# Optimization experiments

Measured on AMD Instinct MI355X. Metric: run time of the kernel, lower is better.

## Reference

```python
import jax, jax.numpy as jnp
import numpy as np

MEM = 32      # mem_size == slot_size (required by role/mem einsum contraction)
SLOT = 32
NREAD = 1
NITER = 3
NIN = 3       # num_input
EPS = 1e-8


def _ln(x, g=None, b=None, eps=1e-5):
    m = x.mean(-1, keepdims=True)
    v = x.var(-1, keepdims=True)
    y = (x - m) / jnp.sqrt(v + eps)
    if g is not None:
        y = y * g + b
    return y


def _lstm_layer(x, Wih, Whh, bih, bhh):
    # x: [S, B, Din]; torch gate order i, f, g, o
    B = x.shape[1]
    H = Whh.shape[1]
    def step(carry, xt):
        h, c = carry
        z = xt @ Wih.T + h @ Whh.T + bih + bhh
        i, f, g, o = jnp.split(z, 4, axis=-1)
        c = jax.nn.sigmoid(f) * c + jax.nn.sigmoid(i) * jnp.tanh(g)
        h = jax.nn.sigmoid(o) * jnp.tanh(c)
        return (h, c), h
    init = (jnp.zeros((B, H), x.dtype), jnp.zeros((B, H), x.dtype))
    _, hs = jax.lax.scan(step, init, x)
    return hs


def _slot_attention(inp, inp_cat, Wi, bi, Wq, bq, Wk, bk, Wv, bv, lng, lnb,
                    Wm1, bm1, Wm2, bm2, Wsp, bsp):
    # inp: [S, B, NIN, 64]; dropout is identity (eval)
    S, B = inp.shape[0], inp.shape[1]
    init_slots = (inp_cat @ Wi.T + bi).reshape(S, B, -1, SLOT)
    k = jax.nn.elu(inp @ Wk.T + bk) + 1.0
    v = inp @ Wv.T + bv
    slots = init_slots
    for _ in range(NITER):
        q = (slots @ Wq.T + bq + init_slots) * SLOT ** (-0.5)
        q = jax.nn.elu(q) + 1.0
        logits = jnp.einsum('sbik,sbjk->sbij', k, q)
        attn = jax.nn.softmax(logits, axis=3) + EPS
        attn = attn / attn.sum(axis=2, keepdims=True)
        upd = jnp.einsum('sbij,sbik->sbjk', attn, v)
        h = _ln(upd, lng, lnb)
        mlp = jax.nn.relu(h @ Wm1.T + bm1) @ Wm2.T + bm2
        slots = slots + mlp / SLOT
    slots = jnp.concatenate([init_slots, slots], axis=-1)
    return slots @ Wsp.T + bsp


def _mask_read(slots, mask, i):
    return jnp.tanh(jnp.einsum('sbne,n->sbe', slots, jnp.roll(mask, i)))


def setup_inputs() -> dict:
    key = jax.random.key(0)
    ks = jax.random.split(key, 20)
    def n(k, shape):
        return jax.random.normal(k, shape, jnp.float32) * 0.05
    z = lambda s: jnp.zeros(s, jnp.float32)
    return {
        'tokens': jax.random.randint(ks[0], (512, 64), 0, 32000),
        'embed_W': n(ks[1], (32000, 256)),
        'Wih0': n(ks[2], (2048, 256)), 'Whh0': n(ks[3], (2048, 512)),
        'bih0': z(2048), 'bhh0': z(2048),
        'Wih1': n(ks[4], (2048, 512)), 'Whh1': n(ks[5], (2048, 512)),
        'bih1': z(2048), 'bhh1': z(2048),
        'Wpi': n(ks[6], (192, 256)), 'bpi': z(192),
        'Wq': n(ks[7], (32, 32)), 'bq': z(32),
        'Wk': n(ks[8], (32, 64)), 'bk': z(32),
        'Wv': n(ks[9], (32, 64)), 'bv': z(32),
        'lng': jnp.ones(32, jnp.float32), 'lnb': z(32),
        'Wm1': n(ks[10], (64, 32)), 'bm1': z(64),
        'Wm2': n(ks[11], (32, 64)), 'bm2': z(32),
        'Wbind': n(ks[12], (96, 192)), 'bbind': z(96),
        'Wreas': n(ks[13], (64, 192)), 'breas': z(64),
        'Wsp': n(ks[14], (32, 64)), 'bsp': z(32),
        'Wg': n(ks[15], (1, 512)), 'bg': z(1),
        'Wout': n(ks[16], (128, 544)), 'bout': z(128),
    }


def reference(tokens, embed_W, Wih0, Whh0, bih0, bhh0, Wih1, Whh1, bih1, bhh1,
              Wpi, bpi, Wq, bq, Wk, bk, Wv, bv, lng, lnb, Wm1, bm1, Wm2, bm2,
              Wbind, bbind, Wreas, breas, Wsp, bsp, Wg, bg, Wout, bout):
    S, B = tokens.shape
    emb = embed_W[tokens]                                   # [S,B,256]
    h = _lstm_layer(emb, Wih0, Whh0, bih0, bhh0)            # [S,B,512]
    h = _lstm_layer(h, Wih1, Whh1, bih1, bhh1)
    dec_in = (emb @ Wpi.T + bpi).reshape(S, B, NIN, -1)     # [S,B,3,64]
    dec_cat = dec_in.reshape(S, B, -1)
    sa = (Wq, bq, Wk, bk, Wv, bv, lng, lnb, Wm1, bm1, Wm2, bm2, Wsp, bsp)
    bind_slots = _slot_attention(dec_in, dec_cat, Wbind, bbind, *sa)  # [S,B,3,32]
    reas_slots = _slot_attention(dec_in, dec_cat, Wreas, breas, *sa)  # [S,B,2,32]
    e = 1e-6
    mask_b = jnp.array([1.0 - 2 * e, e, e], emb.dtype)
    role1 = _mask_read(bind_slots, mask_b, 0)
    role2 = _mask_read(bind_slots, mask_b, 1)
    filler = _mask_read(bind_slots, mask_b, 2)
    mask_r = jnp.array([1.0 - (1 + NREAD) * e, e], emb.dtype)
    u1 = _mask_read(reas_slots, mask_r, 0)
    u2 = _mask_read(reas_slots, mask_r, 1)
    gate = jax.nn.sigmoid(h @ Wg.T + bg + 1.0)              # [S,B,1]

    def step(mem, xs):
        r1, r2, f, g_t, u1t, u2t = xs
        role = jnp.einsum('br,bt->brt', r1, r2)
        prev = jnp.einsum('brt,brtf->bf', role, mem)
        cur = g_t * (f - prev)
        mem = mem + jnp.einsum('brt,bf->brtf', role, cur / MEM)
        nrm = jnp.sqrt(jnp.sum(mem * mem, axis=(1, 2, 3)))
        nrm = jax.nn.relu(nrm - 1.0) + 1.0
        mem = mem / nrm[:, None, None, None]
        read = _ln(jnp.einsum('bsrv,bs,br->bv', mem, u1t, u2t))
        return mem, read

    mem0 = jnp.zeros((B, MEM, MEM, MEM), emb.dtype)
    _, reads = jax.lax.scan(step, mem0, (role1, role2, filler, gate, u1, u2))
    out = jnp.concatenate([h, reads], axis=-1) @ Wout.T + bout
    return out
```

## Files before the change

### kernel.cpp

```cpp
#include <hip/hip_runtime.h>

typedef unsigned short u16;
typedef unsigned int u32;
typedef unsigned long long u64;
typedef __bf16 bf16x8 __attribute__((ext_vector_type(8)));
typedef float f32x4 __attribute__((ext_vector_type(4)));

__device__ __forceinline__ float bf2f(u16 u) { return __uint_as_float(((u32)u) << 16); }
__device__ __forceinline__ u16 f2bf(float f) {
    u32 u = __float_as_uint(f);
    u32 r = (u + 0x7FFFu + ((u >> 16) & 1u)) >> 16;
    return (u16)r;
}
__device__ __forceinline__ float sigm(float x) { return 1.0f / (1.0f + __expf(-x)); }
__device__ __forceinline__ float elu1(float x) { return x > 0.0f ? x + 1.0f : __expf(x); }

__device__ __forceinline__ int ag_load(const int* p) {
    return __hip_atomic_load(p, __ATOMIC_RELAXED, __HIP_MEMORY_SCOPE_AGENT);
}
__device__ __forceinline__ void ag_store(int* p, int v) {
    __hip_atomic_store(p, v, __ATOMIC_RELAXED, __HIP_MEMORY_SCOPE_AGENT);
}
__device__ __forceinline__ void llc_store2(u16* p, u16 a, u16 b) {
    u32 v = (u32)a | ((u32)b << 16);
    __hip_atomic_store((u32*)p, v, __ATOMIC_RELAXED, __HIP_MEMORY_SCOPE_AGENT);
}
__device__ __forceinline__ void llc_store_u16(u16* p, u16 v) {
    __hip_atomic_store(p, v, __ATOMIC_RELAXED, __HIP_MEMORY_SCOPE_AGENT);
}

struct Cvt8 { const float* s[8]; u16* d[8]; int off4[9]; };

__global__ __launch_bounds__(256) void k_f2b8(Cvt8 c)
{
    int i = blockIdx.x * 256 + threadIdx.x;
    if (i >= c.off4[8]) return;
    int k = 0;
#pragma unroll
    for (int q = 1; q < 8; q++) if (i >= c.off4[q]) k = q;
    int j = i - c.off4[k];
    float4 v = ((const float4*)c.s[k])[j];
    ushort4 o;
    o.x = f2bf(v.x); o.y = f2bf(v.y); o.z = f2bf(v.z); o.w = f2bf(v.w);
    ((ushort4*)c.d[k])[j] = o;
}

__global__ __launch_bounds__(256) void k_embed(const int* __restrict__ tok,
                                               const float* __restrict__ W,
                                               u16* __restrict__ out)
{
    int c = blockIdx.x * 256 + threadIdx.x;
    int row = c >> 5, cc = (c & 31) * 8;
    int t = tok[row];
    const float* src = W + (size_t)t * 256 + cc;
    u16 tmp[8];
#pragma unroll
    for (int k = 0; k < 8; k++) tmp[k] = f2bf(src[k]);
    *(uint4*)(out + (size_t)row * 256 + cc) = *(uint4*)tmp;
}

__global__ __launch_bounds__(256) void k_gemm_bt(
    const u16* __restrict__ A, int lda,
    const u16* __restrict__ B,
    u16* __restrict__ Cb, float* __restrict__ Cf, int ldc,
    const float* __restrict__ bias1, const float* __restrict__ bias2,
    int N, int K)
{
    __shared__ u16 As[128][40];
    __shared__ u16 Bs[128][40];
    const int tid = threadIdx.x;
    const int m0 = blockIdx.x * 128, n0 = blockIdx.y * 128;
    const int wave = tid >> 6, lane = tid & 63;
    const int wm = wave & 1, wn = wave >> 1;
    const int quad = lane >> 4, l16 = lane & 15;
    f32x4 acc[4][4] = {};
    for (int k0 = 0; k0 < K; k0 += 32) {
        __syncthreads();
#pragma unroll
        for (int i = 0; i < 2; i++) {
            int c = tid + i * 256, row = c >> 2, cc = (c & 3) * 8;
            *(uint4*)(&As[row][cc]) = *(const uint4*)(A + (size_t)(m0 + row) * lda + k0 + cc);
            uint4 d = {0, 0, 0, 0};
            if (n0 + row < N) d = *(const uint4*)(B + (size_t)(n0 + row) * K + k0 + cc);
            *(uint4*)(&Bs[row][cc]) = d;
        }
        __syncthreads();
        bf16x8 af[4], bfm[4];
#pragma unroll
        for (int x = 0; x < 4; x++) {
            af[x]  = *(const bf16x8*)(&As[wm * 64 + x * 16 + l16][quad * 8]);
            bfm[x] = *(const bf16x8*)(&Bs[wn * 64 + x * 16 + l16][quad * 8]);
        }
#pragma unroll
        for (int mi = 0; mi < 4; mi++)
#pragma unroll
            for (int ni = 0; ni < 4; ni++)
                acc[mi][ni] = __builtin_amdgcn_mfma_f32_16x16x32_bf16(af[mi], bfm[ni], acc[mi][ni], 0, 0, 0);
    }
#pragma unroll
    for (int ni = 0; ni < 4; ni++) {
        int col = n0 + wn * 64 + ni * 16 + l16;
        if (col < N) {
            float bv = 0.f;
            if (bias1) bv += bias1[col];
            if (bias2) bv += bias2[col];
#pragma unroll
            for (int mi = 0; mi < 4; mi++) {
                int r0 = m0 + wm * 64 + mi * 16 + quad * 4;
#pragma unroll
                for (int r = 0; r < 4; r++) {
                    float v = acc[mi][ni][r] + bv;
                    if (Cb) Cb[(size_t)(r0 + r) * ldc + col] = f2bf(v);
                    else    Cf[(size_t)(r0 + r) * ldc + col] = v;
                }
            }
        }
    }
}

template <int NSLOT>
__global__ __launch_bounds__(256) void k_slot(
    const u16* __restrict__ dec, const u16* __restrict__ initp,
    const float* __restrict__ Wq, const float* __restrict__ bq,
    const float* __restrict__ Wk, const float* __restrict__ bk,
    const float* __restrict__ Wv, const float* __restrict__ bv,
    const float* __restrict__ lng, const float* __restrict__ lnb,
    const float* __restrict__ Wm1, const float* __restrict__ bm1,
    const float* __restrict__ Wm2, const float* __restrict__ bm2,
    const float* __restrict__ Wsp, const float* __restrict__ bsp,
    float* __restrict__ o1, float* __restrict__ o2, float* __restrict__ o3)
{
    __shared__ float WqT[32][33], WkT[64][33], WvT[64][33], Wm1T[32][65], Wm2T[64][33], WspT[64][33];
    __shared__ float bq_s[32], bk_s[32], bv_s[32], bm1_s[64], bm2_s[32], bsp_s[32], g_s[32], be_s[32];
    __shared__ u16 xbuf[8][192];
    __shared__ float slots[8][3][32], initl[8][3][32], kk[8][3][32], vv[8][3][32], qq[8][3][32];
    __shared__ float att[8][3][4];
    __shared__ float ubuf[8][32];
    __shared__ float hid[8][64];
    const int tid = threadIdx.x;
    for (int i = tid; i < 1024; i += 256) { int o = i >> 5, c = i & 31; WqT[c][o] = Wq[o * 32 + c]; }
    for (int i = tid; i < 2048; i += 256) {
        int o6 = i >> 6, c6 = i & 63;
        WkT[c6][o6]  = Wk[o6 * 64 + c6];
        WvT[c6][o6]  = Wv[o6 * 64 + c6];
        Wm2T[c6][o6] = Wm2[o6 * 64 + c6];
        WspT[c6][o6] = Wsp[o6 * 64 + c6];
        int o5 = i >> 5, c5 = i & 31;
        Wm1T[c5][o5] = Wm1[o5 * 32 + c5];
    }
    if (tid < 32) {
        bq_s[tid] = bq[tid]; bk_s[tid] = bk[tid]; bv_s[tid] = bv[tid];
        bm2_s[tid] = bm2[tid]; bsp_s[tid] = bsp[tid];
        g_s[tid] = lng[tid]; be_s[tid] = lnb[tid];
    }
    if (tid < 64) bm1_s[tid] = bm1[tid];
    const int p = tid >> 5, l = tid & 31;
    const size_t row = (size_t)blockIdx.x * 8 + p;
    for (int i = l; i < 192; i += 32) xbuf[p][i] = dec[row * 192 + i];
    __syncthreads();
#pragma unroll
    for (int i = 0; i < 3; i++) {
        float aK = bk_s[l], aV = bv_s[l];
        for (int c = 0; c < 64; c++) {
            float x = bf2f(xbuf[p][i * 64 + c]);
            aK += x * WkT[c][l];
            aV += x * WvT[c][l];
        }
        kk[p][i][l] = elu1(aK);
        vv[p][i][l] = aV;
    }
#pragma unroll
    for (int j = 0; j < NSLOT; j++) {
        float iv = bf2f(initp[row * (NSLOT * 32) + j * 32 + l]);
        initl[p][j][l] = iv;
        slots[p][j][l] = iv;
    }
    __syncthreads();
    const float rs = 0.17677669529663687f;
    for (int it = 0; it < 3; it++) {
#pragma unroll
        for (int j = 0; j < NSLOT; j++) {
            float a = bq_s[l];
            for (int c = 0; c < 32; c++) a += slots[p][j][c] * WqT[c][l];
            qq[p][j][l] = elu1((a + initl[p][j][l]) * rs);
        }
        __syncthreads();
        if (l < 3 * NSLOT) {
            int i = l / NSLOT, j = l % NSLOT;
            float s = 0.f;
            for (int c = 0; c < 32; c++) s += kk[p][i][c] * qq[p][j][c];
            att[p][i][j] = s;
        }
        __syncthreads();
        if (l < 3) {
            float mx = -1e30f;
            for (int j = 0; j < NSLOT; j++) mx = fmaxf(mx, att[p][l][j]);
            float sm = 0.f, ex[NSLOT];
            for (int j = 0; j < NSLOT; j++) { ex[j] = __expf(att[p][l][j] - mx); sm += ex[j]; }
            for (int j = 0; j < NSLOT; j++) att[p][l][j] = ex[j] / sm + 1e-8f;
        }
        __syncthreads();
        if (l < NSLOT) {
            float s = att[p][0][l] + att[p][1][l] + att[p][2][l];
            float inv = 1.0f / s;
            for (int i = 0; i < 3; i++) att[p][i][l] *= inv;
        }
        __syncthreads();
#pragma unroll
        for (int j = 0; j < NSLOT; j++) {
            float u = att[p][0][j] * vv[p][0][l] + att[p][1][j] * vv[p][1][l] + att[p][2][j] * vv[p][2][l];
            float mean = u;
            for (int mk = 1; mk < 32; mk <<= 1) mean += __shfl_xor(mean, mk, 32);
            mean *= (1.0f / 32.0f);
            float d = u - mean;
            float var = d * d;
            for (int mk = 1; mk < 32; mk <<= 1) var += __shfl_xor(var, mk, 32);
            var *= (1.0f / 32.0f);
            float y = d * rsqrtf(var + 1e-5f) * g_s[l] + be_s[l];
            ubuf[p][l] = y;
            __syncthreads();
#pragma unroll
            for (int oo = 0; oo < 2; oo++) {
                int o = l + oo * 32;
                float a = bm1_s[o];
                for (int c = 0; c < 32; c++) a += ubuf[p][c] * Wm1T[c][o];
                hid[p][o] = fmaxf(a, 0.f);
            }
            __syncthreads();
            float a2 = bm2_s[l];
            for (int c = 0; c < 64; c++) a2 += hid[p][c] * Wm2T[c][l];
            slots[p][j][l] += a2 * (1.0f / 32.0f);
            __syncthreads();
        }
    }
    float pj[NSLOT];
#pragma unroll
    for (int j = 0; j < NSLOT; j++) {
        float a = bsp_s[l];
        for (int c = 0; c < 32; c++) a += initl[p][j][c] * WspT[c][l];
        for (int c = 0; c < 32; c++) a += slots[p][j][c] * WspT[32 + c][l];
        pj[j] = a;
    }
    const float e = 1e-6f, me = (float)(1.0 - 2e-6);
    if (NSLOT == 3) {
        o1[row * 32 + l] = tanhf(me * pj[0] + e * pj[1] + e * pj[2]);
        o2[row * 32 + l] = tanhf(e * pj[0] + me * pj[1] + e * pj[2]);
        o3[row * 32 + l] = tanhf(e * pj[0] + e * pj[1] + me * pj[2]);
    } else {
        o1[row * 32 + l] = tanhf(me * pj[0] + e * pj[1]);
        o2[row * 32 + l] = tanhf(e * pj[0] + me * pj[1]);
    }
}

__global__ __launch_bounds__(256) void k_mega(
    const u16* __restrict__ emb,
    const u16* __restrict__ Wx0, const u16* __restrict__ Wh0,
    const u16* __restrict__ Wx1, const u16* __restrict__ Wh1,
    const float* __restrict__ bi0, const float* __restrict__ bh0,
    const float* __restrict__ bi1, const float* __restrict__ bh1,
    u16* __restrict__ h0seq,
    u16* __restrict__ h1seq,
    u16* __restrict__ acat,
    int* __restrict__ flags,
    const float* __restrict__ r1, const float* __restrict__ r2,
    const float* __restrict__ fi, const float* __restrict__ uu1,
    const float* __restrict__ uu2,
    const float* __restrict__ Wg, const float* __restrict__ bg)
{
    const int tid = threadIdx.x;
    const int blk = blockIdx.x;
    int* f0  = flags;
    int* f1  = flags + 4096;
    int* f1s = flags + 8192;

    if (blk < 128) {
        __shared__ u16 Wx[32][528];
        __shared__ u16 Wh[32][528];
        __shared__ float zs[4][16][33];
        const int layer = blk >> 6;
        const int me = blk & 63;
        const int jbase = me * 8;
        const int Kx = layer ? 512 : 256;
        const u16* Wxp = layer ? Wx1 : Wx0;
        const u16* Whp = layer ? Wh1 : Wh0;
        const float* bi = layer ? bi1 : bi0;
        const float* bh = layer ? bh1 : bh0;
#pragma unroll
        for (int i = 0; i < 8; i++) {
            int c = tid + i * 256;
            int row = c >> 6, cc = (c & 63) * 8;
            int grow = (row >> 3) * 512 + jbase + (row & 7);
            *(uint4*)(&Wh[row][cc]) = *(const uint4*)(Whp + (size_t)grow * 512 + cc);
        }
        {
            int cpr = Kx >> 3;
            int iters = (32 * cpr) >> 8;
            for (int i = 0; i < iters; i++) {
                int c = tid + i * 256;
                int row = c / cpr, cc = (c % cpr) * 8;
                int grow = (row >> 3) * 512 + jbase + (row & 7);
                *(uint4*)(&Wx[row][cc]) = *(const uint4*)(Wxp + (size_t)grow * Kx + cc);
            }
        }
        const int wave = tid >> 6, lane = tid & 63;
        const int quad = lane >> 4, l16 = lane & 15;
        const int m = wave * 16 + l16;
        const int bl = lane >> 2;
        const int b = wave * 16 + bl;
        const int jj = (lane & 3) * 2;
        const int hoff = quad * 512 + m * 8;
        float bia0[4], bia1[4];
#pragma unroll
        for (int g = 0; g < 4; g++) {
            bia0[g] = bi[g * 512 + jbase + jj]     + bh[g * 512 + jbase + jj];
            bia1[g] = bi[g * 512 + jbase + jj + 1] + bh[g * 512 + jbase + jj + 1];
        }
        const int pollOwn = (wave * 64 + lane) * 16;
        const int pubIdx  = (wave * 64 + me) * 16;
        float c0 = 0.f, c1 = 0.f;
        __syncthreads();
        for (int t = 0; t < 512; t++) {
            f32x4 acc0 = {}, acc1 = {};
            if (!layer) {
                const u16* xrow = emb + ((size_t)t * 64 + m) * 256;
#pragma unroll
                for (int kc = 0; kc < 8; kc++) {
                    bf16x8 a  = *(const bf16x8*)(xrow + kc * 32 + quad * 8);
                    bf16x8 w0 = *(const bf16x8*)(&Wx[l16][kc * 32 + quad * 8]);
                    bf16x8 w1 = *(const bf16x8*)(&Wx[16 + l16][kc * 32 + quad * 8]);
                    acc0 = __builtin_amdgcn_mfma_f32_16x16x32_bf16(a, w0, acc0, 0, 0, 0);
                    acc1 = __builtin_amdgcn_mfma_f32_16x16x32_bf16(a, w1, acc1, 0, 0, 0);
                }
                if (t > 0) {
                    int it = 0;
                    for (;;) {
                        int a = ag_load(f0 + pollOwn);
                        if (__all(a >= t)) break;
                        if (++it > 3000000) break;
                        __builtin_amdgcn_s_sleep(1);
                    }
                    const u16* hrd = h0seq + (size_t)(t - 1) * 32768 + hoff;
#pragma unroll
                    for (int kc = 0; kc < 16; kc++) {
                        bf16x8 a  = *(const bf16x8*)(hrd + kc * 2048);
                        bf16x8 w0 = *(const bf16x8*)(&Wh[l16][kc * 32 + quad * 8]);
                        bf16x8 w1 = *(const bf16x8*)(&Wh[16 + l16][kc * 32 + quad * 8]);
                        acc0 = __builtin_amdgcn_mfma_f32_16x16x32_bf16(a, w0, acc0, 0, 0, 0);
                        acc1 = __builtin_amdgcn_mfma_f32_16x16x32_bf16(a, w1, acc1, 0, 0, 0);
                    }
                }
            } else {
                {
                    int it = 0;
                    for (;;) {
                        int a = ag_load(f0 + pollOwn);
                        if (__all(a >= t + 1)) break;
                        if (++it > 3000000) break;
                        __builtin_amdgcn_s_sleep(1);
                    }
                }
                const u16* xrow = h0seq + (size_t)t * 32768 + hoff;
#pragma unroll
                for (int kc = 0; kc < 16; kc++) {
                    bf16x8 a  = *(const bf16x8*)(xrow + kc * 2048);
                    bf16x8 w0 = *(const bf16x8*)(&Wx[l16][kc * 32 + quad * 8]);
                    bf16x8 w1 = *(const bf16x8*)(&Wx[16 + l16][kc * 32 + quad * 8]);
                    acc0 = __builtin_amdgcn_mfma_f32_16x16x32_bf16(a, w0, acc0, 0, 0, 0);
                    acc1 = __builtin_amdgcn_mfma_f32_16x16x32_bf16(a, w1, acc1, 0, 0, 0);
                }
                if (t > 0) {
                    int it = 0;
                    for (;;) {
                        int a = ag_load(f1 + pollOwn);
                        if (__all(a >= t)) break;
                        if (++it > 3000000) break;
                        __builtin_amdgcn_s_sleep(1);
                    }
                    const u16* hrd = h1seq + (size_t)(t - 1) * 32768 + hoff;
#pragma unroll
                    for (int kc = 0; kc < 16; kc++) {
                        bf16x8 a  = *(const bf16x8*)(hrd + kc * 2048);
                        bf16x8 w0 = *(const bf16x8*)(&Wh[l16][kc * 32 + quad * 8]);
                        bf16x8 w1 = *(const bf16x8*)(&Wh[16 + l16][kc * 32 + quad * 8]);
                        acc0 = __builtin_amdgcn_mfma_f32_16x16x32_bf16(a, w0, acc0, 0, 0, 0);
                        acc1 = __builtin_amdgcn_mfma_f32_16x16x32_bf16(a, w1, acc1, 0, 0, 0);
                    }
                }
            }
#pragma unroll
            for (int r = 0; r < 4; r++) {
                zs[wave][quad * 4 + r][l16]      = acc0[r];
                zs[wave][quad * 4 + r][16 + l16] = acc1[r];
            }
            u16 hb0, hb1;
            {
                float zi0 = zs[wave][bl][jj]      + bia0[0];
                float zf0 = zs[wave][bl][8 + jj]  + bia0[1];
                float zg0 = zs[wave][bl][16 + jj] + bia0[2];
                float zo0 = zs[wave][bl][24 + jj] + bia0[3];
                c0 = sigm(zf0) * c0 + sigm(zi0) * tanhf(zg0);
                float h0v = sigm(zo0) * tanhf(c0);
                float zi1 = zs[wave][bl][jj + 1]      + bia1[0];
                float zf1 = zs[wave][bl][8 + jj + 1]  + bia1[1];
                float zg1 = zs[wave][bl][16 + jj + 1] + bia1[2];
                float zo1 = zs[wave][bl][24 + jj + 1] + bia1[3];
                c1 = sigm(zf1) * c1 + sigm(zi1) * tanhf(zg1);
                float h1v = sigm(zo1) * tanhf(c1);
                hb0 = f2bf(h0v); hb1 = f2bf(h1v);
            }
            if (!layer) {
                llc_store2(h0seq + (size_t)t * 32768 + me * 512 + b * 8 + jj, hb0, hb1);
                __builtin_amdgcn_s_waitcnt(0);
                if (lane == 0) ag_store(f0 + pubIdx, t + 1);
            } else {
                llc_store2(h1seq + (size_t)t * 32768 + me * 512 + b * 8 + jj, hb0, hb1);
                __builtin_amdgcn_s_waitcnt(0);
                if (lane == 0) ag_store(f1 + pubIdx, t + 1);
                llc_store2(acat + ((size_t)t * 64 + b) * 544 + jbase + jj, hb0, hb1);
                __builtin_amdgcn_s_waitcnt(0);
                if (lane == 0) ag_store(f1s + pubIdx, t + 1);
            }
        }
    } else {
        const int sb = blk - 128;
        const int grp = sb >> 4;
        const int f = tid & 31, rg = tid >> 5;
        float m[4][32];
#pragma unroll
        for (int x = 0; x < 4; x++)
            for (int y = 0; y < 32; y++) m[x][y] = 0.f;
        __shared__ float r1s[32], r2s[32], fis[32], u1s[32], u2s[32];
        __shared__ float red[8][32];
        __shared__ float wred[4];
        __shared__ float gpart[4];
        float wg0 = Wg[2 * tid], wg1 = Wg[2 * tid + 1];
        float bgv = bg[0];
        for (int t = 0; t < 512; t++) {
            float pre = 0.f;
            {
                size_t base = ((size_t)t * 64 + sb) * 32;
                if (tid < 32) pre = r1[base + tid];
                else if (tid < 64) pre = r2[base + tid - 32];
                else if (tid < 96) pre = fi[base + tid - 64];
                else if (tid < 128) pre = uu1[base + tid - 96];
                else if (tid < 160) pre = uu2[base + tid - 128];
            }
            if (tid < 64) {
                int* p1 = f1s + (grp * 64 + tid) * 16;
                int it = 0;
                for (;;) {
                    int a = ag_load(p1);
                    if (__all(a >= t + 1)) break;
                    if (++it > 3000000) break;
                    __builtin_amdgcn_s_sleep(1);
                }
            }
            __syncthreads();
            if (tid < 32) r1s[tid] = pre;
            else if (tid < 64) r2s[tid - 32] = pre;
            else if (tid < 96) fis[tid - 64] = pre;
            else if (tid < 128) u1s[tid - 96] = pre;
            else if (tid < 160) u2s[tid - 128] = pre;
            {
                const u16* hr = acat + ((size_t)t * 64 + sb) * 544;
                u32 hv = *(const u32*)(hr + 2 * tid);
                float gp = bf2f((u16)hv) * wg0 + bf2f((u16)(hv >> 16)) * wg1;
                for (int mk = 1; mk < 64; mk <<= 1) gp += __shfl_xor(gp, mk, 64);
                if ((tid & 63) == 0) gpart[tid >> 6] = gp;
            }
            __syncthreads();
            float gsh = sigm(gpart[0] + gpart[1] + gpart[2] + gpart[3] + bgv + 1.0f);
            float p = 0.f;
#pragma unroll
            for (int rl = 0; rl < 4; rl++) {
                float s = 0.f;
                for (int ti = 0; ti < 32; ti++) s += r2s[ti] * m[rl][ti];
                p += r1s[rg * 4 + rl] * s;
            }
            red[rg][f] = p;
            __syncthreads();
            float prev = 0.f;
#pragma unroll
            for (int g = 0; g < 8; g++) prev += red[g][f];
            float curo = gsh * (fis[f] - prev) * (1.0f / 32.0f);
            float nsq = 0.f;
#pragma unroll
            for (int rl = 0; rl < 4; rl++) {
                float a = r1s[rg * 4 + rl] * curo;
                for (int ti = 0; ti < 32; ti++) {
                    m[rl][ti] += a * r2s[ti];
                    nsq += m[rl][ti] * m[rl][ti];
                }
            }
            for (int mk = 1; mk < 64; mk <<= 1) nsq += __shfl_xor(nsq, mk, 64);
            __syncthreads();
            if ((tid & 63) == 0) wred[tid >> 6] = nsq;
            __syncthreads();
            float nrm = sqrtf(wred[0] + wred[1] + wred[2] + wred[3]);
            float sc = nrm > 1.0f ? 1.0f / nrm : 1.0f;
            float rp = 0.f;
#pragma unroll
            for (int rl = 0; rl < 4; rl++) {
                float s = 0.f;
                for (int ti = 0; ti < 32; ti++) {
                    m[rl][ti] *= sc;
                    s += m[rl][ti] * u2s[ti];
                }
                rp += u1s[rg * 4 + rl] * s;
            }
            red[rg][f] = rp;
            __syncthreads();
            float rv = 0.f;
#pragma unroll
            for (int g = 0; g < 8; g++) rv += red[g][f];
            float mean = rv;
            for (int mk = 1; mk < 32; mk <<= 1) mean += __shfl_xor(mean, mk, 32);
            mean *= (1.0f / 32.0f);
            float d = rv - mean;
            float var = d * d;
            for (int mk = 1; mk < 32; mk <<= 1) var += __shfl_xor(var, mk, 32);
            var *= (1.0f / 32.0f);
            if (tid < 32) {
                float y = d * rsqrtf(var + 1e-5f);
                llc_store_u16(acat + ((size_t)t * 64 + sb) * 544 + 512 + f, f2bf(y));
            }
            __syncthreads();
        }
    }
}

extern "C" void kernel_launch(void* const* d_in, const int* in_sizes, int n_in,
                              void* d_out, int out_size, void* d_ws, size_t ws_size,
                              hipStream_t stream)
{
    (void)in_sizes; (void)n_in; (void)out_size; (void)ws_size;
    const int*   tokens = (const int*)d_in[0];
    const float* embW  = (const float*)d_in[1];
    const float* Wih0  = (const float*)d_in[2];
    const float* Whh0  = (const float*)d_in[3];
    const float* bih0  = (const float*)d_in[4];
    const float* bhh0  = (const float*)d_in[5];
    const float* Wih1  = (const float*)d_in[6];
    const float* Whh1  = (const float*)d_in[7];
    const float* bih1  = (const float*)d_in[8];
    const float* bhh1  = (const float*)d_in[9];
    const float* Wpi   = (const float*)d_in[10];
    const float* bpi   = (const float*)d_in[11];
    const float* Wq    = (const float*)d_in[12];
    const float* bq    = (const float*)d_in[13];
    const float* Wk    = (const float*)d_in[14];
    const float* bk    = (const float*)d_in[15];
    const float* Wv    = (const float*)d_in[16];
    const float* bv    = (const float*)d_in[17];
    const float* lng   = (const float*)d_in[18];
    const float* lnb   = (const float*)d_in[19];
    const float* Wm1   = (const float*)d_in[20];
    const float* bm1   = (const float*)d_in[21];
    const float* Wm2   = (const float*)d_in[22];
    const float* bm2   = (const float*)d_in[23];
    const float* Wbind = (const float*)d_in[24];
    const float* bbind = (const float*)d_in[25];
    const float* Wreas = (const float*)d_in[26];
    const float* breas = (const float*)d_in[27];
    const float* Wsp   = (const float*)d_in[28];
    const float* bsp   = (const float*)d_in[29];
    const float* Wg    = (const float*)d_in[30];
    const float* bg    = (const float*)d_in[31];
    const float* Wout  = (const float*)d_in[32];
    const float* bout  = (const float*)d_in[33];

    char* ws = (char*)d_ws;
    size_t off = 0;
    auto alloc = [&](size_t bytes) { size_t o = off; off += (bytes + 255) & ~(size_t)255; return o; };
    int*  flags  = (int*)(ws + alloc(16384 * 4));
    u16*  emb    = (u16*)(ws + alloc(32768ull * 256 * 2));
    u16*  dec    = (u16*)(ws + alloc(32768ull * 192 * 2));
    u16*  initb  = (u16*)(ws + alloc(32768ull * 96 * 2));
    u16*  initr  = (u16*)(ws + alloc(32768ull * 64 * 2));
    u16*  acat   = (u16*)(ws + alloc(32768ull * 544 * 2));
    u16*  h0seq  = (u16*)(ws + alloc(512ull * 64 * 512 * 2));
    u16*  h1seq  = (u16*)(ws + alloc(512ull * 64 * 512 * 2));
    float* role1 = (float*)(ws + alloc(32768ull * 32 * 4));
    float* role2 = (float*)(ws + alloc(32768ull * 32 * 4));
    float* fill  = (float*)(ws + alloc(32768ull * 32 * 4));
    float* u1v   = (float*)(ws + alloc(32768ull * 32 * 4));
    float* u2v   = (float*)(ws + alloc(32768ull * 32 * 4));
    u16* Wx0b  = (u16*)(ws + alloc(2048ull * 256 * 2));
    u16* Wh0b  = (u16*)(ws + alloc(2048ull * 512 * 2));
    u16* Wx1b  = (u16*)(ws + alloc(2048ull * 512 * 2));
    u16* Wh1b  = (u16*)(ws + alloc(2048ull * 512 * 2));
    u16* Wpib  = (u16*)(ws + alloc(192ull * 256 * 2));
    u16* Wbindb = (u16*)(ws + alloc(96ull * 192 * 2));
    u16* Wreasb = (u16*)(ws + alloc(64ull * 192 * 2));
    u16* Woutb  = (u16*)(ws + alloc(128ull * 544 * 2));

    hipMemsetAsync(flags, 0, 16384 * 4, stream);
    {
        Cvt8 c;
        const float* s[8] = {Wih0, Whh0, Wih1, Whh1, Wpi, Wbind, Wreas, Wout};
        u16* d[8] = {Wx0b, Wh0b, Wx1b, Wh1b, Wpib, Wbindb, Wreasb, Woutb};
        int n[8] = {2048 * 256, 2048 * 512, 2048 * 512, 2048 * 512,
                    192 * 256, 96 * 192, 64 * 192, 128 * 544};
        int acc = 0;
        for (int k = 0; k < 8; k++) { c.s[k] = s[k]; c.d[k] = d[k]; c.off4[k] = acc; acc += n[k] / 4; }
        c.off4[8] = acc;
        k_f2b8<<<(acc + 255) / 256, 256, 0, stream>>>(c);
    }
    k_embed<<<4096, 256, 0, stream>>>(tokens, embW, emb);
    k_gemm_bt<<<dim3(256, 2), 256, 0, stream>>>(emb, 256, Wpib, dec, nullptr, 192, bpi, nullptr, 192, 256);
    k_gemm_bt<<<dim3(256, 1), 256, 0, stream>>>(dec, 192, Wbindb, initb, nullptr, 96, bbind, nullptr, 96, 192);
    k_gemm_bt<<<dim3(256, 1), 256, 0, stream>>>(dec, 192, Wreasb, initr, nullptr, 64, breas, nullptr, 64, 192);
    k_slot<3><<<4096, 256, 0, stream>>>(dec, initb, Wq, bq, Wk, bk, Wv, bv, lng, lnb,
                                        Wm1, bm1, Wm2, bm2, Wsp, bsp, role1, role2, fill);
    k_slot<2><<<4096, 256, 0, stream>>>(dec, initr, Wq, bq, Wk, bk, Wv, bv, lng, lnb,
                                        Wm1, bm1, Wm2, bm2, Wsp, bsp, u1v, u2v, nullptr);
    k_mega<<<192, 256, 0, stream>>>(emb, Wx0b, Wh0b, Wx1b, Wh1b,
                                    bih0, bhh0, bih1, bhh1,
                                    h0seq, h1seq, acat, flags,
                                    role1, role2, fill, u1v, u2v, Wg, bg);
    k_gemm_bt<<<dim3(256, 1), 256, 0, stream>>>(acat, 544, Woutb, nullptr, (float*)d_out, 128, bout, nullptr, 128, 544);
}
```

Baseline: 3.526 ms.

## Compact flag layout, merge layer-1 flags, and split MFMA accumulator chains

Flags are packed densely (no 64-byte padding per flag), and layer 1 now publishes one flag, after both its h1 and acat stores, instead of two. Layer-1 blocks poll the layer-0 and layer-1 flags in a single combined loop before starting their step. The MFMA loops are unrolled by two with four independent accumulators, which shortens dependency chains. The denser flags may suffer false sharing when writers hit the same cache line, and merging the polls delays the input GEMM until the recurrent dependency is also ready.

```diff
diff --git a/kernel.cpp b/kernel.cpp
--- a/kernel.cpp
+++ b/kernel.cpp
@@ -269,9 +269,8 @@
 {
     const int tid = threadIdx.x;
     const int blk = blockIdx.x;
-    int* f0  = flags;
-    int* f1  = flags + 4096;
-    int* f1s = flags + 8192;
+    int* f0 = flags;
+    int* f1 = flags + 256;
 
     if (blk < 128) {
         __shared__ u16 Wx[32][528];
@@ -315,78 +314,79 @@
             bia0[g] = bi[g * 512 + jbase + jj]     + bh[g * 512 + jbase + jj];
             bia1[g] = bi[g * 512 + jbase + jj + 1] + bh[g * 512 + jbase + jj + 1];
         }
-        const int pollOwn = (wave * 64 + lane) * 16;
-        const int pubIdx  = (wave * 64 + me) * 16;
+        int* pollF0 = f0 + wave * 64 + lane;
+        int* pollF1 = f1 + wave * 64 + lane;
+        int* pubF   = (layer ? f1 : f0) + wave * 64 + me;
         float c0 = 0.f, c1 = 0.f;
         __syncthreads();
         for (int t = 0; t < 512; t++) {
-            f32x4 acc0 = {}, acc1 = {};
+            f32x4 acc0 = {}, acc1 = {}, acc2 = {}, acc3 = {};
             if (!layer) {
                 const u16* xrow = emb + ((size_t)t * 64 + m) * 256;
 #pragma unroll
-                for (int kc = 0; kc < 8; kc++) {
-                    bf16x8 a  = *(const bf16x8*)(xrow + kc * 32 + quad * 8);
-                    bf16x8 w0 = *(const bf16x8*)(&Wx[l16][kc * 32 + quad * 8]);
-                    bf16x8 w1 = *(const bf16x8*)(&Wx[16 + l16][kc * 32 + quad * 8]);
-                    acc0 = __builtin_amdgcn_mfma_f32_16x16x32_bf16(a, w0, acc0, 0, 0, 0);
-                    acc1 = __builtin_amdgcn_mfma_f32_16x16x32_bf16(a, w1, acc1, 0, 0, 0);
+                for (int kc = 0; kc < 8; kc += 2) {
+                    bf16x8 a0 = *(const bf16x8*)(xrow + kc * 32 + quad * 8);
+                    bf16x8 a1 = *(const bf16x8*)(xrow + (kc + 1) * 32 + quad * 8);
+                    acc0 = __builtin_amdgcn_mfma_f32_16x16x32_bf16(a0, *(const bf16x8*)(&Wx[l16][kc * 32 + quad * 8]), acc0, 0, 0, 0);
+                    acc1 = __builtin_amdgcn_mfma_f32_16x16x32_bf16(a0, *(const bf16x8*)(&Wx[16 + l16][kc * 32 + quad * 8]), acc1, 0, 0, 0);
+                    acc2 = __builtin_amdgcn_mfma_f32_16x16x32_bf16(a1, *(const bf16x8*)(&Wx[l16][(kc + 1) * 32 + quad * 8]), acc2, 0, 0, 0);
+                    acc3 = __builtin_amdgcn_mfma_f32_16x16x32_bf16(a1, *(const bf16x8*)(&Wx[16 + l16][(kc + 1) * 32 + quad * 8]), acc3, 0, 0, 0);
                 }
                 if (t > 0) {
                     int it = 0;
                     for (;;) {
-                        int a = ag_load(f0 + pollOwn);
+                        int a = ag_load(pollF0);
                         if (__all(a >= t)) break;
                         if (++it > 3000000) break;
                         __builtin_amdgcn_s_sleep(1);
                     }
                     const u16* hrd = h0seq + (size_t)(t - 1) * 32768 + hoff;
 #pragma unroll
-                    for (int kc = 0; kc < 16; kc++) {
-                        bf16x8 a  = *(const bf16x8*)(hrd + kc * 2048);
-                        bf16x8 w0 = *(const bf16x8*)(&Wh[l16][kc * 32 + quad * 8]);
-                        bf16x8 w1 = *(const bf16x8*)(&Wh[16 + l16][kc * 32 + quad * 8]);
-                        acc0 = __builtin_amdgcn_mfma_f32_16x16x32_bf16(a, w0, acc0, 0, 0, 0);
-                        acc1 = __builtin_amdgcn_mfma_f32_16x16x32_bf16(a, w1, acc1, 0, 0, 0);
+                    for (int kc = 0; kc < 16; kc += 2) {
+                        bf16x8 a0 = *(const bf16x8*)(hrd + kc * 2048);
+                        bf16x8 a1 = *(const bf16x8*)(hrd + (kc + 1) * 2048);
+                        acc0 = __builtin_amdgcn_mfma_f32_16x16x32_bf16(a0, *(const bf16x8*)(&Wh[l16][kc * 32 + quad * 8]), acc0, 0, 0, 0);
+                        acc1 = __builtin_amdgcn_mfma_f32_16x16x32_bf16(a0, *(const bf16x8*)(&Wh[16 + l16][kc * 32 + quad * 8]), acc1, 0, 0, 0);
+                        acc2 = __builtin_amdgcn_mfma_f32_16x16x32_bf16(a1, *(const bf16x8*)(&Wh[l16][(kc + 1) * 32 + quad * 8]), acc2, 0, 0, 0);
+                        acc3 = __builtin_amdgcn_mfma_f32_16x16x32_bf16(a1, *(const bf16x8*)(&Wh[16 + l16][(kc + 1) * 32 + quad * 8]), acc3, 0, 0, 0);
                     }
                 }
             } else {
                 {
                     int it = 0;
                     for (;;) {
-                        int a = ag_load(f0 + pollOwn);
-                        if (__all(a >= t + 1)) break;
+                        int a0 = ag_load(pollF0);
+                        int a1 = ag_load(pollF1);
+                        if (__all((a0 >= t + 1) && (a1 >= t))) break;
                         if (++it > 3000000) break;
                         __builtin_amdgcn_s_sleep(1);
                     }
                 }
                 const u16* xrow = h0seq + (size_t)t * 32768 + hoff;
 #pragma unroll
-                for (int kc = 0; kc < 16; kc++) {
-                    bf16x8 a  = *(const bf16x8*)(xrow + kc * 2048);
-                    bf16x8 w0 = *(const bf16x8*)(&Wx[l16][kc * 32 + quad * 8]);
-                    bf16x8 w1 = *(const bf16x8*)(&Wx[16 + l16][kc * 32 + quad * 8]);
-                    acc0 = __builtin_amdgcn_mfma_f32_16x16x32_bf16(a, w0, acc0, 0, 0, 0);
-                    acc1 = __builtin_amdgcn_mfma_f32_16x16x32_bf16(a, w1, acc1, 0, 0, 0);
+                for (int kc = 0; kc < 16; kc += 2) {
+                    bf16x8 a0 = *(const bf16x8*)(xrow + kc * 2048);
+                    bf16x8 a1 = *(const bf16x8*)(xrow + (kc + 1) * 2048);
+                    acc0 = __builtin_amdgcn_mfma_f32_16x16x32_bf16(a0, *(const bf16x8*)(&Wx[l16][kc * 32 + quad * 8]), acc0, 0, 0, 0);
+                    acc1 = __builtin_amdgcn_mfma_f32_16x16x32_bf16(a0, *(const bf16x8*)(&Wx[16 + l16][kc * 32 + quad * 8]), acc1, 0, 0, 0);
+                    acc2 = __builtin_amdgcn_mfma_f32_16x16x32_bf16(a1, *(const bf16x8*)(&Wx[l16][(kc + 1) * 32 + quad * 8]), acc2, 0, 0, 0);
+                    acc3 = __builtin_amdgcn_mfma_f32_16x16x32_bf16(a1, *(const bf16x8*)(&Wx[16 + l16][(kc + 1) * 32 + quad * 8]), acc3, 0, 0, 0);
                 }
                 if (t > 0) {
-                    int it = 0;
-                    for (;;) {
-                        int a = ag_load(f1 + pollOwn);
-                        if (__all(a >= t)) break;
-                        if (++it > 3000000) break;
-                        __builtin_amdgcn_s_sleep(1);
+                    const u16* hrd = h1seq + (size_t)(t - 1) * 32768 + hoff;
+#pragma unroll
+                    for (int kc = 0; kc < 16; kc += 2) {
+                        bf16x8 a0 = *(const bf16x8*)(hrd + kc * 2048);
+                        bf16x8 a1 = *(const bf16x8*)(hrd + (kc + 1) * 2048);
+                        acc0 = __builtin_amdgcn_mfma_f32_16x16x32_bf16(a0, *(const bf16x8*)(&Wh[l16][kc * 32 + quad * 8]), acc0, 0, 0, 0);
+                        acc1 = __builtin_amdgcn_mfma_f32_16x16x32_bf16(a0, *(const bf16x8*)(&Wh[16 + l16][kc * 32 + quad * 8]), acc1, 0, 0, 0);
+                        acc2 = __builtin_amdgcn_mfma_f32_16x16x32_bf16(a1, *(const bf16x8*)(&Wh[l16][(kc + 1) * 32 + quad * 8]), acc2, 0, 0, 0);
+                        acc3 = __builtin_amdgcn_mfma_f32_16x16x32_bf16(a1, *(const bf16x8*)(&Wh[16 + l16][(kc + 1) * 32 + quad * 8]), acc3, 0, 0, 0);
                     }
-                    const u16* hrd = h1seq + (size_t)(t - 1) * 32768 + hoff;
-#pragma unroll
-                    for (int kc = 0; kc < 16; kc++) {
-                        bf16x8 a  = *(const bf16x8*)(hrd + kc * 2048);
-                        bf16x8 w0 = *(const bf16x8*)(&Wh[l16][kc * 32 + quad * 8]);
-                        bf16x8 w1 = *(const bf16x8*)(&Wh[16 + l16][kc * 32 + quad * 8]);
-                        acc0 = __builtin_amdgcn_mfma_f32_16x16x32_bf16(a, w0, acc0, 0, 0, 0);
-                        acc1 = __builtin_amdgcn_mfma_f32_16x16x32_bf16(a, w1, acc1, 0, 0, 0);
-                    }
-                }
-            }
+                }
+            }
+            acc0[0] += acc2[0]; acc0[1] += acc2[1]; acc0[2] += acc2[2]; acc0[3] += acc2[3];
+            acc1[0] += acc3[0]; acc1[1] += acc3[1]; acc1[2] += acc3[2]; acc1[3] += acc3[3];
 #pragma unroll
             for (int r = 0; r < 4; r++) {
                 zs[wave][quad * 4 + r][l16]      = acc0[r];
@@ -411,14 +411,12 @@
             if (!layer) {
                 llc_store2(h0seq + (size_t)t * 32768 + me * 512 + b * 8 + jj, hb0, hb1);
                 __builtin_amdgcn_s_waitcnt(0);
-                if (lane == 0) ag_store(f0 + pubIdx, t + 1);
+                if (lane == 0) ag_store(pubF, t + 1);
             } else {
                 llc_store2(h1seq + (size_t)t * 32768 + me * 512 + b * 8 + jj, hb0, hb1);
-                __builtin_amdgcn_s_waitcnt(0);
-                if (lane == 0) ag_store(f1 + pubIdx, t + 1);
                 llc_store2(acat + ((size_t)t * 64 + b) * 544 + jbase + jj, hb0, hb1);
                 __builtin_amdgcn_s_waitcnt(0);
-                if (lane == 0) ag_store(f1s + pubIdx, t + 1);
+                if (lane == 0) ag_store(pubF, t + 1);
             }
         }
     } else {
@@ -435,6 +433,7 @@
         __shared__ float gpart[4];
         float wg0 = Wg[2 * tid], wg1 = Wg[2 * tid + 1];
         float bgv = bg[0];
+        const int* pollS = f1 + grp * 64 + (tid & 63);
         for (int t = 0; t < 512; t++) {
             float pre = 0.f;
             {
@@ -446,10 +445,9 @@
                 else if (tid < 160) pre = uu2[base + tid - 128];
             }
             if (tid < 64) {
-                int* p1 = f1s + (grp * 64 + tid) * 16;
                 int it = 0;
                 for (;;) {
-                    int a = ag_load(p1);
+                    int a = ag_load(pollS);
                     if (__all(a >= t + 1)) break;
                     if (++it > 3000000) break;
                     __builtin_amdgcn_s_sleep(1);
```

Measured after the change: 6.642 ms. 1.88x slower.

## Add aggregator block that folds per-producer flags into per-wave epoch counters

Applied to the files above, without the earlier changes.

Adds a 193rd block that spins on all per-producer progress flags, reduces them with a min across the wave, and publishes one epoch counter per wave group. Consumer waves in the LSTM and memory blocks then poll a single shared word instead of each lane loading 64 separate flags and doing a wave vote. This is meant to cut L2/atomic polling traffic on the per-timestep critical path. The cost is an extra hop of latency through the aggregator, plus one spinning block that must be co-resident with the others.

```diff
diff --git a/kernel.cpp b/kernel.cpp
--- a/kernel.cpp
+++ b/kernel.cpp
@@ -272,6 +272,7 @@
     int* f0  = flags;
     int* f1  = flags + 4096;
     int* f1s = flags + 8192;
+    int* eps = flags + 12288;
 
     if (blk < 128) {
         __shared__ u16 Wx[32][528];
@@ -315,8 +316,9 @@
             bia0[g] = bi[g * 512 + jbase + jj]     + bh[g * 512 + jbase + jj];
             bia1[g] = bi[g * 512 + jbase + jj + 1] + bh[g * 512 + jbase + jj + 1];
         }
-        const int pollOwn = (wave * 64 + lane) * 16;
-        const int pubIdx  = (wave * 64 + me) * 16;
+        const int* ep0w = eps + wave * 16;
+        const int* ep1w = eps + (4 + wave) * 16;
+        int* pubF = (layer ? f1 : f0) + (wave * 64 + me) * 16;
         float c0 = 0.f, c1 = 0.f;
         __syncthreads();
         for (int t = 0; t < 512; t++) {
@@ -334,8 +336,8 @@
                 if (t > 0) {
                     int it = 0;
                     for (;;) {
-                        int a = ag_load(f0 + pollOwn);
-                        if (__all(a >= t)) break;
+                        int a = ag_load(ep0w);
+                        if (a >= t) break;
                         if (++it > 3000000) break;
                         __builtin_amdgcn_s_sleep(1);
                     }
@@ -353,8 +355,8 @@
                 {
                     int it = 0;
                     for (;;) {
-                        int a = ag_load(f0 + pollOwn);
-                        if (__all(a >= t + 1)) break;
+                        int a = ag_load(ep0w);
+                        if (a >= t + 1) break;
                         if (++it > 3000000) break;
                         __builtin_amdgcn_s_sleep(1);
                     }
@@ -371,8 +373,8 @@
                 if (t > 0) {
                     int it = 0;
                     for (;;) {
-                        int a = ag_load(f1 + pollOwn);
-                        if (__all(a >= t)) break;
+                        int a = ag_load(ep1w);
+                        if (a >= t) break;
                         if (++it > 3000000) break;
                         __builtin_amdgcn_s_sleep(1);
                     }
@@ -411,17 +413,17 @@
             if (!layer) {
                 llc_store2(h0seq + (size_t)t * 32768 + me * 512 + b * 8 + jj, hb0, hb1);
                 __builtin_amdgcn_s_waitcnt(0);
-                if (lane == 0) ag_store(f0 + pubIdx, t + 1);
+                if (lane == 0) ag_store(pubF, t + 1);
             } else {
                 llc_store2(h1seq + (size_t)t * 32768 + me * 512 + b * 8 + jj, hb0, hb1);
                 __builtin_amdgcn_s_waitcnt(0);
-                if (lane == 0) ag_store(f1 + pubIdx, t + 1);
+                if (lane == 0) ag_store(pubF, t + 1);
                 llc_store2(acat + ((size_t)t * 64 + b) * 544 + jbase + jj, hb0, hb1);
                 __builtin_amdgcn_s_waitcnt(0);
-                if (lane == 0) ag_store(f1s + pubIdx, t + 1);
-            }
-        }
-    } else {
+                if (lane == 0) ag_store(f1s + (wave * 64 + me) * 16, t + 1);
+            }
+        }
+    } else if (blk < 192) {
         const int sb = blk - 128;
         const int grp = sb >> 4;
         const int f = tid & 31, rg = tid >> 5;
@@ -435,6 +437,7 @@
         __shared__ float gpart[4];
         float wg0 = Wg[2 * tid], wg1 = Wg[2 * tid + 1];
         float bgv = bg[0];
+        const int* epsg = eps + (8 + grp) * 16;
         for (int t = 0; t < 512; t++) {
             float pre = 0.f;
             {
@@ -446,11 +449,10 @@
                 else if (tid < 160) pre = uu2[base + tid - 128];
             }
             if (tid < 64) {
-                int* p1 = f1s + (grp * 64 + tid) * 16;
                 int it = 0;
                 for (;;) {
-                    int a = ag_load(p1);
-                    if (__all(a >= t + 1)) break;
+                    int a = ag_load(epsg);
+                    if (a >= t + 1) break;
                     if (++it > 3000000) break;
                     __builtin_amdgcn_s_sleep(1);
                 }
@@ -525,6 +527,34 @@
                 llc_store_u16(acat + ((size_t)t * 64 + sb) * 544 + 512 + f, f2bf(y));
             }
             __syncthreads();
+        }
+    } else {
+        const int wave = tid >> 6, lane = tid & 63;
+        const int* l0 = f0  + (wave * 64 + lane) * 16;
+        const int* l1 = f1  + (wave * 64 + lane) * 16;
+        const int* l2 = f1s + (wave * 64 + lane) * 16;
+        int* ep0 = eps + wave * 16;
+        int* ep1 = eps + (4 + wave) * 16;
+        int* ep2 = eps + (8 + wave) * 16;
+        int e0 = 0, e1 = 0, e2 = 0;
+        long it = 0;
+        while (e0 < 512 || e1 < 512 || e2 < 512) {
+            if (e0 < 512) {
+                int v = ag_load(l0);
+                for (int mk = 1; mk < 64; mk <<= 1) { int o = __shfl_xor(v, mk, 64); v = v < o ? v : o; }
+                if (v > e0) { if (lane == 0) ag_store(ep0, v); e0 = v; }
+            }
+            if (e1 < 512) {
+                int v = ag_load(l1);
+                for (int mk = 1; mk < 64; mk <<= 1) { int o = __shfl_xor(v, mk, 64); v = v < o ? v : o; }
+                if (v > e1) { if (lane == 0) ag_store(ep1, v); e1 = v; }
+            }
+            if (e2 < 512) {
+                int v = ag_load(l2);
+                for (int mk = 1; mk < 64; mk <<= 1) { int o = __shfl_xor(v, mk, 64); v = v < o ? v : o; }
+                if (v > e2) { if (lane == 0) ag_store(ep2, v); e2 = v; }
+            }
+            if (++it > 50000000) break;
         }
     }
 }
@@ -614,7 +644,7 @@
                                         Wm1, bm1, Wm2, bm2, Wsp, bsp, role1, role2, fill);
     k_slot<2><<<4096, 256, 0, stream>>>(dec, initr, Wq, bq, Wk, bk, Wv, bv, lng, lnb,
                                         Wm1, bm1, Wm2, bm2, Wsp, bsp, u1v, u2v, nullptr);
-    k_mega<<<192, 256, 0, stream>>>(emb, Wx0b, Wh0b, Wx1b, Wh1b,
+    k_mega<<<193, 256, 0, stream>>>(emb, Wx0b, Wh0b, Wx1b, Wh1b,
                                     bih0, bhh0, bih1, bhh1,
                                     h0seq, h1seq, acat, flags,
                                     role1, role2, fill, u1v, u2v, Wg, bg);
```

Result: no change. 3.565 ms (+1.1%).
